# Performance work log

Hardware: AMD Instinct MI355X
Metric: run time of the kernel (lower is better)

The kernel has to match this reference:

```python
import jax, jax.numpy as jnp
import numpy as np


def setup_inputs() -> dict:
    key = jax.random.key(0)
    ks = jax.random.split(key, 9)
    U, H, R, N = 32, 5120, 160, 16
    return {
        "x": jax.random.normal(ks[0], (U, H), jnp.float32),
        "W_delta": jax.random.normal(ks[1], (H, R), jnp.float32) * 0.02,
        "W_dt": jax.random.normal(ks[2], (R, H), jnp.float32) * 0.02,
        "b_dt": jax.random.normal(ks[3], (H,), jnp.float32) * 0.02,
        "W_B": jax.random.normal(ks[4], (H, N), jnp.float32) * 0.02,
        "W_C": jax.random.normal(ks[5], (H, N), jnp.float32) * 0.02,
        "A_log": jax.random.uniform(ks[6], (H, N), jnp.float32),
        "D": jax.random.normal(ks[7], (H,), jnp.float32),
        "h": jax.random.normal(ks[8], (U, H, N), jnp.float32),
    }


def reference(x, W_delta, W_dt, b_dt, W_B, W_C, A_log, D, h):
    # x: (U,H) single-token decode for U users; h: (U,H,N) recurrent state.
    # delta: low-rank projection then dt_proj, softplus
    dt = jax.nn.softplus((x @ W_delta) @ W_dt + b_dt)          # (U,H)
    A = -jnp.exp(A_log)                                        # (H,N)
    abar = jnp.exp(dt[:, :, None] * A[None, :, :])             # (U,H,N)
    B = x @ W_B                                                # (U,N)
    C = x @ W_C                                                # (U,N)
    # state update: h' = abar*h + (dt*B)*x
    h_new = abar * h + dt[:, :, None] * B[:, None, :] * x[:, :, None]  # (U,H,N)
    # output mix: y = C . h' + D*x
    y = jnp.einsum("uhn,un->uh", h_new, C) + x * D[None, :]    # (U,H)
    return y
```

## Files before the change

kernel.cpp:

```cpp
#include <hip/hip_runtime.h>
#include <math.h>

#define UU 32
#define HH 5120
#define RR 160
#define NN 16


#define TMP_WS 0
#define BP_WS  81920
#define CP_WS  90112

__device__ __forceinline__ unsigned short f2bf(float f) {
    unsigned int u = __float_as_uint(f);
    u += 0x7fffu + ((u >> 16) & 1u);
    return (unsigned short)(u >> 16);
}
__device__ __forceinline__ float blo(unsigned int v) { return __uint_as_float(v << 16); }
__device__ __forceinline__ float bhi(unsigned int v) { return __uint_as_float(v & 0xffff0000u); }

__global__ __launch_bounds__(256) void proj_kernel(
    const float* __restrict__ x, const float* __restrict__ Wd,
    const float* __restrict__ WB, const float* __restrict__ WC,
    float* __restrict__ ws)
{
    __shared__ float xs[32 * 36];
    __shared__ float wt[32 * 32];

    const int b = blockIdx.x;
    const int t = threadIdx.x;

    if (b < 80) {
        const int s  = b & 15;
        const int rt = b >> 4;
        const int r0 = rt * 32;
        const int u0 = (t >> 5) * 4;
        const int r  = t & 31;
        float acc[4] = {0.f, 0.f, 0.f, 0.f};

        for (int c = 0; c < 10; c++) {
            const int k0 = s * 320 + c * 32;
            if (c) __syncthreads();
            #pragma unroll
            for (int i = 0; i < 4; i++) {
                int idx = t + i * 256;
                int u = idx >> 5, kk = idx & 31;
                xs[kk * 36 + u] = x[u * HH + k0 + kk];
            }
            {
                int kk = t >> 3, c4 = t & 7;
                *(float4*)&wt[kk * 32 + c4 * 4] =
                    *(const float4*)(Wd + (size_t)(k0 + kk) * RR + r0 + c4 * 4);
            }
            __syncthreads();

            #pragma unroll
            for (int kk = 0; kk < 32; kk++) {
                float4 xv = *(const float4*)&xs[kk * 36 + u0];
                float wv = wt[kk * 32 + r];
                acc[0] += xv.x * wv; acc[1] += xv.y * wv;
                acc[2] += xv.z * wv; acc[3] += xv.w * wv;
            }
        }
        #pragma unroll
        for (int i = 0; i < 4; i++)
            ws[TMP_WS + s * 5120 + (u0 + i) * 160 + r0 + r] = acc[i];
    } else {
        const int sb = b - 80;
        const int k0 = sb * 320;
        const int n  = t & 15;
        const int uu = t >> 4;
        const float* xa = x + uu * HH + k0;
        const float* xb = x + (uu + 16) * HH + k0;
        float aB0 = 0.f, aB1 = 0.f, aC0 = 0.f, aC1 = 0.f;
        #pragma unroll 2
        for (int k4 = 0; k4 < 80; k4++) {
            float4 va = *(const float4*)(xa + k4 * 4);
            float4 vb = *(const float4*)(xb + k4 * 4);
            const int kb = (k0 + k4 * 4) * NN + n;
            #define STEP(D, CMP) { \
                float wb = WB[kb + (D) * NN]; \
                float wc = WC[kb + (D) * NN]; \
                aB0 += va.CMP * wb; aB1 += vb.CMP * wb; \
                aC0 += va.CMP * wc; aC1 += vb.CMP * wc; }
            STEP(0, x) STEP(1, y) STEP(2, z) STEP(3, w)
            #undef STEP
        }
        ws[BP_WS + sb * 512 + uu * 16 + n]        = aB0;
        ws[BP_WS + sb * 512 + (uu + 16) * 16 + n] = aB1;
        ws[CP_WS + sb * 512 + uu * 16 + n]        = aC0;
        ws[CP_WS + sb * 512 + (uu + 16) * 16 + n] = aC1;
    }
}

__device__ __forceinline__ float softplusf(float v) {
    return (v > 20.f) ? v : log1pf(expf(v));
}

__global__ __launch_bounds__(512) void ssm_kernel(
    const float* __restrict__ x, const float* __restrict__ Wdt,
    const float* __restrict__ bdt, const float* __restrict__ Alog,
    const float* __restrict__ Dv, const float* __restrict__ hstate,
    const float* __restrict__ ws, float* __restrict__ y)
{
    __shared__ unsigned short tmp_b[32 * 168];
    __shared__ unsigned short wsl_b[16 * 168];
    __shared__ float Bl[32 * 20];
    __shared__ float Cl[32 * 20];
    __shared__ float an_l[16 * 20];
    __shared__ float xl[32 * 17];
    __shared__ float bdtl[16];
    __shared__ float Dl[16];

    const int t  = threadIdx.x;
    const int h0 = blockIdx.x * 16;
    const int u  = t >> 4;
    const int q  = t & 15;

    const float* hb = hstate + (size_t)(u * HH + h0 + q) * 16;
    float4 hv[4];
    #pragma unroll
    for (int k = 0; k < 4; k++) hv[k] = ((const float4*)hb)[k];

    #pragma unroll
    for (int i = 0; i < 3; i++) {
        int idx4 = t + i * 512;
        if (idx4 < 1280) {
            float sx = 0.f, sy = 0.f, sz = 0.f, sw = 0.f;
            #pragma unroll
            for (int s = 0; s < 16; s++) {
                float4 v = ((const float4*)(ws + TMP_WS + s * 5120))[idx4];
                sx += v.x; sy += v.y; sz += v.z; sw += v.w;
            }
            int uu = idx4 / 40, r4 = idx4 % 40;
            unsigned int p0 = (unsigned int)f2bf(sx) | ((unsigned int)f2bf(sy) << 16);
            unsigned int p1 = (unsigned int)f2bf(sz) | ((unsigned int)f2bf(sw) << 16);
            *(uint2*)&tmp_b[uu * 168 + r4 * 4] = make_uint2(p0, p1);
        }
    }
    #pragma unroll
    for (int i = 0; i < 5; i++) {
        int idx = t + i * 512;
        int r = idx >> 4, hh = idx & 15;
        wsl_b[hh * 168 + r] = f2bf(Wdt[r * HH + h0 + hh]);
    }
    {
        int uu = t >> 4, n = t & 15;
        float sb = 0.f, sc = 0.f;
        #pragma unroll
        for (int s = 0; s < 16; s++) {
            sb += ws[BP_WS + s * 512 + t];
            sc += ws[CP_WS + s * 512 + t];
        }
        Bl[uu * 20 + n] = sb;
        Cl[uu * 20 + n] = sc;
        xl[uu * 17 + n] = x[uu * HH + h0 + n];
    }
    if (t < 256) {
        int hh = t >> 4, n = t & 15;
        an_l[hh * 20 + n] = -expf(Alog[(h0 + hh) * 16 + n]);
    }
    if (t < 16) { bdtl[t] = bdt[h0 + t]; Dl[t] = Dv[h0 + t]; }
    __syncthreads();

    const uint4* ta = (const uint4*)&tmp_b[u * 168];
    const uint4* wp = (const uint4*)&wsl_b[q * 168];
    float ae = 0.f, ao = 0.f;
    #pragma unroll
    for (int c = 0; c < 20; c++) {
        uint4 av = ta[c];
        uint4 wv = wp[c];
        #define MAC(X) \
            ae += blo(av.X) * blo(wv.X); ao += bhi(av.X) * bhi(wv.X);
        MAC(x) MAC(y) MAC(z) MAC(w)
        #undef MAC
    }
    const float dt = softplusf(bdtl[q] + (ae + ao));

    const float xv = xl[u * 17 + q];
    const float K  = dt * xv;
    float yv = xv * Dl[q];
    #pragma unroll
    for (int qq = 0; qq < 4; qq++) {
        float4 h4 = hv[qq];
        float4 b4 = *(const float4*)&Bl[u * 20 + qq * 4];
        float4 c4 = *(const float4*)&Cl[u * 20 + qq * 4];
        float4 a4 = *(const float4*)&an_l[q * 20 + qq * 4];
        yv += (expf(dt * a4.x) * h4.x + K * b4.x) * c4.x;
        yv += (expf(dt * a4.y) * h4.y + K * b4.y) * c4.y;
        yv += (expf(dt * a4.z) * h4.z + K * b4.z) * c4.z;
        yv += (expf(dt * a4.w) * h4.w + K * b4.w) * c4.w;
    }
    y[u * HH + h0 + q] = yv;
}

extern "C" void kernel_launch(void* const* d_in, const int* in_sizes, int n_in,
                              void* d_out, int out_size, void* d_ws, size_t ws_size,
                              hipStream_t stream) {
    const float* x    = (const float*)d_in[0];
    const float* Wd   = (const float*)d_in[1];
    const float* Wdt  = (const float*)d_in[2];
    const float* bdt  = (const float*)d_in[3];
    const float* WB   = (const float*)d_in[4];
    const float* WC   = (const float*)d_in[5];
    const float* Alog = (const float*)d_in[6];
    const float* Dv   = (const float*)d_in[7];
    const float* hst  = (const float*)d_in[8];
    float* y  = (float*)d_out;
    float* ws = (float*)d_ws;

    proj_kernel<<<96, 256, 0, stream>>>(x, Wd, WB, WC, ws);
    ssm_kernel<<<320, 512, 0, stream>>>(x, Wdt, bdt, Alog, Dv, hst, ws, y);
}
```

Baseline: 108.6 us.

## Restructure projection kernel: more blocks, full x tile in LDS, double-buffered weights

The low-rank projection part now launches 160 blocks of 512 threads, each handling a 16-column slice of W_delta over a 320-wide K slab. It loads the whole x slab into shared memory once and double-buffers W_delta chunks through registers, so global loads overlap with compute. The B/C projection blocks stage W_B/W_C tiles in shared memory and give each thread one user instead of two. The aim is more parallelism and less serialized global latency, at the cost of more shared memory per block, lower arithmetic intensity per thread, and x being re-read by more blocks.

```diff
diff --git a/kernel.cpp b/kernel.cpp
--- a/kernel.cpp
+++ b/kernel.cpp
@@ -19,77 +19,88 @@
 __device__ __forceinline__ float blo(unsigned int v) { return __uint_as_float(v << 16); }
 __device__ __forceinline__ float bhi(unsigned int v) { return __uint_as_float(v & 0xffff0000u); }
 
-__global__ __launch_bounds__(256) void proj_kernel(
+#define XS_STRIDE 324
+
+__global__ __launch_bounds__(512) void proj_kernel(
     const float* __restrict__ x, const float* __restrict__ Wd,
     const float* __restrict__ WB, const float* __restrict__ WC,
     float* __restrict__ ws)
 {
-    __shared__ float xs[32 * 36];
-    __shared__ float wt[32 * 32];
+    __shared__ float smem[32 * XS_STRIDE + 2 * 512];
 
     const int b = blockIdx.x;
     const int t = threadIdx.x;
 
-    if (b < 80) {
+    if (b < 160) {
+        float* xs = smem;
+        float (*wt)[512] = (float(*)[512])(smem + 32 * XS_STRIDE);
         const int s  = b & 15;
         const int rt = b >> 4;
-        const int r0 = rt * 32;
-        const int u0 = (t >> 5) * 4;
-        const int r  = t & 31;
-        float acc[4] = {0.f, 0.f, 0.f, 0.f};
-
-        for (int c = 0; c < 10; c++) {
-            const int k0 = s * 320 + c * 32;
-            if (c) __syncthreads();
+        const int r0 = rt * 16;
+        const int kbase = s * 320;
+        const int r = t & 15;
+        const int u = t >> 4;
+
+        #pragma unroll
+        for (int i = 0; i < 5; i++) {
+            int idx4 = t + i * 512;
+            int uu = idx4 / 80, k4 = idx4 % 80;
+            *(float4*)&xs[uu * XS_STRIDE + k4 * 4] =
+                *(const float4*)(x + uu * HH + kbase + k4 * 4);
+        }
+        float4 wreg;
+        if (t < 128) {
+            int kk = t >> 2, c4 = t & 3;
+            wreg = *(const float4*)(Wd + (size_t)(kbase + kk) * RR + r0 + c4 * 4);
+        }
+
+        float acc = 0.f;
+        int p = 0;
+        for (int c = 0; c < 10; c++, p ^= 1) {
+            if (t < 128)
+                *(float4*)&wt[p][(t >> 2) * 16 + (t & 3) * 4] = wreg;
+            __syncthreads();
+            if (t < 128 && c < 9) {
+                int kk = t >> 2, c4 = t & 3;
+                wreg = *(const float4*)(Wd + (size_t)(kbase + (c + 1) * 32 + kk) * RR + r0 + c4 * 4);
+            }
+            const float* xp = &xs[u * XS_STRIDE + c * 32];
+            const float* wp = &wt[p][r];
             #pragma unroll
-            for (int i = 0; i < 4; i++) {
-                int idx = t + i * 256;
-                int u = idx >> 5, kk = idx & 31;
-                xs[kk * 36 + u] = x[u * HH + k0 + kk];
-            }
-            {
-                int kk = t >> 3, c4 = t & 7;
-                *(float4*)&wt[kk * 32 + c4 * 4] =
-                    *(const float4*)(Wd + (size_t)(k0 + kk) * RR + r0 + c4 * 4);
-            }
-            __syncthreads();
-
-            #pragma unroll
-            for (int kk = 0; kk < 32; kk++) {
-                float4 xv = *(const float4*)&xs[kk * 36 + u0];
-                float wv = wt[kk * 32 + r];
-                acc[0] += xv.x * wv; acc[1] += xv.y * wv;
-                acc[2] += xv.z * wv; acc[3] += xv.w * wv;
-            }
-        }
-        #pragma unroll
-        for (int i = 0; i < 4; i++)
-            ws[TMP_WS + s * 5120 + (u0 + i) * 160 + r0 + r] = acc[i];
+            for (int kk = 0; kk < 32; kk++)
+                acc += xp[kk] * wp[kk * 16];
+        }
+        ws[TMP_WS + s * 5120 + u * 160 + r0 + r] = acc;
     } else {
-        const int sb = b - 80;
+        float* wbl = smem;
+        float* wcl = smem + 320 * 16;
+        const int sb = b - 160;
         const int k0 = sb * 320;
         const int n  = t & 15;
         const int uu = t >> 4;
-        const float* xa = x + uu * HH + k0;
-        const float* xb = x + (uu + 16) * HH + k0;
-        float aB0 = 0.f, aB1 = 0.f, aC0 = 0.f, aC1 = 0.f;
-        #pragma unroll 2
+
+        #pragma unroll
+        for (int i = 0; i < 3; i++) {
+            int idx4 = t + i * 512;
+            if (idx4 < 1280) {
+                ((float4*)wbl)[idx4] = ((const float4*)(WB + (size_t)k0 * NN))[idx4];
+                ((float4*)wcl)[idx4] = ((const float4*)(WC + (size_t)k0 * NN))[idx4];
+            }
+        }
+        __syncthreads();
+
+        const float* xp = x + uu * HH + k0;
+        float aB = 0.f, aC = 0.f;
+        #pragma unroll 4
         for (int k4 = 0; k4 < 80; k4++) {
-            float4 va = *(const float4*)(xa + k4 * 4);
-            float4 vb = *(const float4*)(xb + k4 * 4);
-            const int kb = (k0 + k4 * 4) * NN + n;
-            #define STEP(D, CMP) { \
-                float wb = WB[kb + (D) * NN]; \
-                float wc = WC[kb + (D) * NN]; \
-                aB0 += va.CMP * wb; aB1 += vb.CMP * wb; \
-                aC0 += va.CMP * wc; aC1 += vb.CMP * wc; }
-            STEP(0, x) STEP(1, y) STEP(2, z) STEP(3, w)
-            #undef STEP
-        }
-        ws[BP_WS + sb * 512 + uu * 16 + n]        = aB0;
-        ws[BP_WS + sb * 512 + (uu + 16) * 16 + n] = aB1;
-        ws[CP_WS + sb * 512 + uu * 16 + n]        = aC0;
-        ws[CP_WS + sb * 512 + (uu + 16) * 16 + n] = aC1;
+            float4 v = *(const float4*)(xp + k4 * 4);
+            const float* wb = &wbl[k4 * 64 + n];
+            const float* wc = &wcl[k4 * 64 + n];
+            aB += v.x * wb[0] + v.y * wb[16] + v.z * wb[32] + v.w * wb[48];
+            aC += v.x * wc[0] + v.y * wc[16] + v.z * wc[32] + v.w * wc[48];
+        }
+        ws[BP_WS + sb * 512 + t] = aB;
+        ws[CP_WS + sb * 512 + t] = aC;
     }
 }
 
@@ -209,6 +220,6 @@
     float* y  = (float*)d_out;
     float* ws = (float*)d_ws;
 
-    proj_kernel<<<96, 256, 0, stream>>>(x, Wd, WB, WC, ws);
+    proj_kernel<<<176, 512, 0, stream>>>(x, Wd, WB, WC, ws);
     ssm_kernel<<<320, 512, 0, stream>>>(x, Wdt, bdt, Alog, Dv, hst, ws, y);
 }
```

After: 168.2 us. 1.55x slower.
